# Performance work log

Hardware: AMD Instinct MI355X
Metric: run time of the kernel (lower is better)

Reference implementation:

```python
import jax, jax.numpy as jnp
import numpy as np

N = 100_000   # nodes
D = 128       # feature dim (dim_in == dim_out, residual requires it)
E = 1_600_000 # edges
T = 4         # num_layers; edge_attr (hop distance) in 1..T


def setup_inputs() -> dict:
    key = jax.random.key(0)
    k0, k1, k2, k3, k4 = jax.random.split(key, 5)
    x = jax.random.normal(k0, (N, D), dtype=jnp.float32)
    edge_index = jax.random.randint(k1, (2, E), 0, N, dtype=jnp.int32)
    edge_attr = jax.random.randint(k2, (E,), 1, T + 1, dtype=jnp.int32)  # hop k in [1, T]
    W = jax.random.normal(k3, (T, D, D), dtype=jnp.float32) * (1.0 / np.sqrt(D))
    nu = jax.random.normal(k4, (T, T), dtype=jnp.float32) * 0.1  # nu[k-1, t]
    return {"x": x, "edge_index": edge_index, "edge_attr": edge_attr, "W": W, "nu": nu}


def _gcn_edge_coef(edge_index, mask, n):
    """Symmetric GCN normalization 1/sqrt(deg_src*deg_dst) restricted to masked edges."""
    src, dst = edge_index[0], edge_index[1]
    deg_s = jax.ops.segment_sum(mask, src, num_segments=n)
    deg_d = jax.ops.segment_sum(mask, dst, num_segments=n)
    inv = lambda d: jnp.where(d > 0, jax.lax.rsqrt(jnp.maximum(d, 1.0)), 0.0)
    return mask * inv(deg_s)[src] * inv(deg_d)[dst]  # [E]


def reference(x, edge_index, edge_attr, W, nu):
    n = x.shape[0]
    T_layers = nu.shape[1]
    src, dst = edge_index[0], edge_index[1]
    # Precompute per-hop normalized edge coefficients (A(k) masks as weights -> static shapes)
    coefs = [_gcn_edge_coef(edge_index, (edge_attr == k).astype(x.dtype), n)
             for k in range(1, T_layers + 1)]
    hist = [x]  # x_t history
    for t in range(T_layers):
        acc = jnp.zeros_like(x)
        for k in range(1, t + 2):  # k = 1 .. t+1
            h = hist[t + 1 - k] @ W[k - 1]                      # [N, D] linear
            msg = h[src] * coefs[k - 1][:, None]                # gather + weight [E, D]
            agg = jax.ops.segment_sum(msg, dst, num_segments=n) # scatter-sum [N, D]
            acc = acc + nu[k - 1, t] * agg
        xt = hist[t] + jax.nn.relu(acc)                         # residual + ReLU
        # F.normalize(p=2, dim=-1), eps=1e-12 (cfg.gnn.l2norm assumed True)
        xt = xt / jnp.maximum(jnp.linalg.norm(xt, axis=-1, keepdims=True), 1e-12)
        hist.append(xt)
    return hist[-1]
```

## Files before the change

kernel.cpp:

```cpp
#include <hip/hip_runtime.h>

#define DD 128
#define NP 256
#define EB 8192

typedef float4 f4;
typedef __attribute__((ext_vector_type(8))) short bf16x8;
typedef __attribute__((ext_vector_type(4))) float f32x4;

__device__ __forceinline__ short toBf(float f) {
    unsigned u = __float_as_uint(f);
    u += 0x7fff + ((u >> 16) & 1);
    return (short)(u >> 16);
}
__device__ __forceinline__ float bf2f(unsigned short u) {
    return __uint_as_float(((unsigned)u) << 16);
}


__global__ __launch_bounds__(1024) void kA(const int* __restrict__ ei, int E, int PSZ, int nbA,
                                           int* __restrict__ cntB_D, int* __restrict__ cntB_S) {
    __shared__ int hd[NP], hs[NP];
    int tid = threadIdx.x;
    if (tid < NP) { hd[tid] = 0; hs[tid] = 0; }
    __syncthreads();
    int base = blockIdx.x * EB;
    int lim = min(base + EB, E);
    for (int e = base + tid; e < lim; e += 1024) {
        int s = ei[e], d = ei[E + e];
        atomicAdd(&hs[s / PSZ], 1);
        atomicAdd(&hd[d / PSZ], 1);
    }
    __syncthreads();
    if (tid < NP) {
        cntB_D[tid * nbA + blockIdx.x] = hd[tid];
        cntB_S[tid * nbA + blockIdx.x] = hs[tid];
    }
}

__global__ __launch_bounds__(512) void kB1(int* __restrict__ cntB_D, int* __restrict__ cntB_S,
                                           int nbA,
                                           int* __restrict__ partTotD, int* __restrict__ partTotS) {
    __shared__ int sh[512];
    int b = blockIdx.x, tid = threadIdx.x;
    int* cntB = (b < NP) ? cntB_D : cntB_S;
    int* partTot = (b < NP) ? partTotD : partTotS;
    int p = (b < NP) ? b : b - NP;
    int v = (tid < nbA) ? cntB[p * nbA + tid] : 0;
    sh[tid] = v; __syncthreads();
    for (int off = 1; off < 512; off <<= 1) {
        int add = (tid >= off) ? sh[tid - off] : 0;
        __syncthreads(); sh[tid] += add; __syncthreads();
    }
    if (tid < nbA) cntB[p * nbA + tid] = sh[tid] - v;
    if (tid == 511) partTot[p] = sh[511];
}

__global__ __launch_bounds__(512) void kB2(const int* __restrict__ partTotD,
                                           const int* __restrict__ partTotS,
                                           int* __restrict__ partStartD,
                                           int* __restrict__ partStartS, int E) {
    __shared__ int sh[512];
    int tid = threadIdx.x;
    bool isD = tid < 256;
    int idx = isD ? tid : tid - 256;
    int v = isD ? partTotD[idx] : partTotS[idx];
    sh[tid] = v; __syncthreads();
    for (int off = 1; off < 256; off <<= 1) {
        int add = (idx >= off) ? sh[tid - off] : 0;
        __syncthreads(); sh[tid] += add; __syncthreads();
    }
    if (isD) partStartD[idx] = sh[tid] - v; else partStartS[idx] = sh[tid] - v;
    if (idx == 255) { if (isD) partStartD[NP] = E; else partStartS[NP] = E; }
}

__global__ __launch_bounds__(1024) void kC(const int* __restrict__ ei, const int* __restrict__ ea,
                                           int E, int N, int T, int PSZ, int nbA,
                                           const int* __restrict__ cntB_D, const int* __restrict__ cntB_S,
                                           const int* __restrict__ partStartD,
                                           const int* __restrict__ partStartS,
                                           int2* __restrict__ binD, int* __restrict__ binS) {
    __shared__ int pd[NP], ps[NP];
    int tid = threadIdx.x, b = blockIdx.x;
    if (tid < NP) {
        pd[tid] = cntB_D[tid * nbA + b] + partStartD[tid];
        ps[tid] = cntB_S[tid * nbA + b] + partStartS[tid];
    }
    __syncthreads();
    int base = b * EB;
    int lim = min(base + EB, E);
    for (int e = base + tid; e < lim; e += 1024) {
        int s = ei[e], d = ei[E + e], k = ea[e] - 1;
        int dp = d / PSZ, sp = s / PSZ;
        int posD = atomicAdd(&pd[dp], 1);
        binD[posD] = make_int2((d - dp * PSZ) * T + k, (k << 26) | (k * N + s));
        int posS = atomicAdd(&ps[sp], 1);
        binS[posS] = (s - sp * PSZ) * T + k;
    }
}

__global__ __launch_bounds__(512) void kDE(const int2* __restrict__ binD,
                                           const int* __restrict__ binS,
                                           const int* __restrict__ partStartD,
                                           const int* __restrict__ partStartS,
                                           int N, int T, int PSZ, int M, int E,
                                           int* __restrict__ rowptr, float* __restrict__ isdD2,
                                           int* __restrict__ ep, float* __restrict__ isdS) {
    __shared__ int cnt[4096];
    __shared__ int part[512];
    int b = blockIdx.x, tid = threadIdx.x;
    int nloc = PSZ * T;
    for (int i = tid; i < nloc; i += 512) cnt[i] = 0;
    __syncthreads();
    if (b < NP) {
        int p = b;
        int b0 = partStartD[p], b1 = partStartD[p + 1];
        for (int e = b0 + tid; e < b1; e += 512) atomicAdd(&cnt[binD[e].x], 1);
        __syncthreads();
        int CH = (nloc + 511) / 512;
        int c0 = tid * CH, c1 = min(c0 + CH, nloc);
        int s = 0;
        for (int i = c0; i < c1; i++) s += cnt[i];
        part[tid] = s; __syncthreads();
        for (int off = 1; off < 512; off <<= 1) {
            int add = (tid >= off) ? part[tid - off] : 0;
            __syncthreads(); part[tid] += add; __syncthreads();
        }
        int run = ((tid == 0) ? 0 : part[tid - 1]) + b0;
        int gb_base = p * PSZ * T;
        for (int i = c0; i < c1; i++) {
            int v = cnt[i];
            cnt[i] = run;
            int gb = gb_base + i;
            if (gb < M) {
                rowptr[gb] = run;
                isdD2[gb] = rsqrtf((float)max(v, 1));
            }
            run += v;
        }
        __syncthreads();
        for (int e = b0 + tid; e < b1; e += 512) {
            int2 v = binD[e];
            int pos = atomicAdd(&cnt[v.x], 1);
            ep[pos] = v.y;
        }
        if (p == 0 && tid == 0) rowptr[M] = E;
    } else {
        int p = b - NP;
        int b0 = partStartS[p], b1 = partStartS[p + 1];
        for (int e = b0 + tid; e < b1; e += 512) atomicAdd(&cnt[binS[e]], 1);
        __syncthreads();
        int s0 = p * PSZ;
        for (int i = tid; i < nloc; i += 512) {
            int sl = i / T, k = i - sl * T;
            int snode = s0 + sl;
            if (snode < N) isdS[k * N + snode] = rsqrtf((float)max(cnt[i], 1));
        }
    }
}

__global__ void k_prepW(const float* __restrict__ W, ushort* __restrict__ WT, int tot) {
    int i = blockIdx.x * blockDim.x + threadIdx.x;
    if (i >= tot) return;
    int k = i >> 14, rem = i & 16383, j = rem >> 7, d = rem & 127;
    WT[i] = (ushort)toBf(W[(size_t)k * 16384 + (size_t)d * DD + j]);
}

__global__ void k_cvt(const float* __restrict__ x, ushort* __restrict__ xb, int n8) {
    int i = blockIdx.x * blockDim.x + threadIdx.x;
    if (i >= n8) return;
    const f4* q = (const f4*)(x + (size_t)i * 8);
    f4 lo = q[0], hi = q[1];
    bf16x8 r;
    r[0] = toBf(lo.x); r[1] = toBf(lo.y); r[2] = toBf(lo.z); r[3] = toBf(lo.w);
    r[4] = toBf(hi.x); r[5] = toBf(hi.y); r[6] = toBf(hi.z); r[7] = toBf(hi.w);
    *(bf16x8*)(xb + (size_t)i * 8) = r;
}


struct APtrs { const ushort* a0; const ushort* a1; const ushort* a2; const ushort* a3; };

__global__ __launch_bounds__(256) void k_gemm_batch(APtrs ap,
                                                    const ushort* __restrict__ WTb,
                                                    const float* __restrict__ iskb,
                                                    ushort* __restrict__ Hb, int N) {
    __shared__ ushort lW[128 * 128];
    int k0 = blockIdx.y;
    const ushort* A = (k0 == 0) ? ap.a0 : (k0 == 1) ? ap.a1 : (k0 == 2) ? ap.a2 : ap.a3;
    const ushort* WT = WTb + (size_t)k0 * DD * DD;
    const float* isk = iskb + (size_t)k0 * N;
    ushort* H = Hb + (size_t)k0 * N * DD;

    int tid = threadIdx.x;
#pragma unroll
    for (int i = 0; i < 8; i++) {
        int g = tid + i * 256;
        int row = g >> 4, slot = g & 15;
        bf16x8 v = *(const bf16x8*)(WT + row * DD + slot * 8);
        *(bf16x8*)(lW + row * DD + (slot ^ (row & 7)) * 8) = v;
    }
    __syncthreads();

    int wave = tid >> 6;
    int lane = tid & 63;
    int rlo = lane & 15;
    int khi = lane >> 4;
    int r0 = blockIdx.x * 256 + wave * 64;

    f32x4 acc[4][8];
#pragma unroll
    for (int s = 0; s < 4; s++)
#pragma unroll
        for (int j = 0; j < 8; j++) acc[s][j] = (f32x4){0.f, 0.f, 0.f, 0.f};

    int ca[4];
#pragma unroll
    for (int s = 0; s < 4; s++) {
        int r = r0 + s * 16 + rlo;
        ca[s] = r < N ? r : N - 1;
    }

#pragma unroll
    for (int kk = 0; kk < 4; kk++) {
        int d0 = kk * 32 + khi * 8;
        bf16x8 a[4];
#pragma unroll
        for (int s = 0; s < 4; s++)
            a[s] = *(const bf16x8*)(A + (size_t)ca[s] * DD + d0);
        int q = kk * 4 + khi;
#pragma unroll
        for (int cg = 0; cg < 8; cg++) {
            int row = cg * 16 + rlo;
            bf16x8 b = *(const bf16x8*)(lW + row * DD + (q ^ (rlo & 7)) * 8);
#pragma unroll
            for (int s = 0; s < 4; s++)
                acc[s][cg] = __builtin_amdgcn_mfma_f32_16x16x32_bf16(a[s], b, acc[s][cg], 0, 0, 0);
        }
    }

#pragma unroll
    for (int s = 0; s < 4; s++) {
#pragma unroll
        for (int r = 0; r < 4; r++) {
            int row = r0 + s * 16 + khi * 4 + r;
            if (row < N) {
                float sc = isk[row];
#pragma unroll
                for (int cg = 0; cg < 8; cg++)
                    H[(size_t)row * DD + cg * 16 + rlo] = (ushort)toBf(sc * acc[s][cg][r]);
            }
        }
    }
}


__device__ __forceinline__ float selw(float w0, float w1, float w2, float w3, int k) {
    float a = (k & 1) ? w1 : w0;
    float b = (k & 1) ? w3 : w2;
    return (k & 2) ? b : a;
}

__global__ __launch_bounds__(256) void k_agg_fin(
        const ushort* __restrict__ H,
        const int* __restrict__ ep,
        const int* __restrict__ rp,
        const float* __restrict__ isdD2,
        const float* __restrict__ nu, int t, int T, int nk,
        const ushort* __restrict__ hp,
        ushort* __restrict__ hnB,
        float* __restrict__ outF,
        int N) {
    int node = (blockIdx.x * blockDim.x + threadIdx.x) >> 5;
    if (node >= N) return;
    int lane = threadIdx.x & 31;
    int rbase = node * T;
    int b0 = rp[rbase], b1 = rp[rbase + nk];

    float w0 = nu[t] * isdD2[rbase];
    float w1 = (1 < nk) ? nu[T + t]     * isdD2[rbase + 1] : 0.f;
    float w2 = (2 < nk) ? nu[2 * T + t] * isdD2[rbase + 2] : 0.f;
    float w3 = (3 < nk) ? nu[3 * T + t] * isdD2[rbase + 3] : 0.f;

    const char* Hc = (const char*)H;
    unsigned lb = (unsigned)lane << 3;

    float sx = 0.f, sy = 0.f, sz = 0.f, sw = 0.f;
    int e = b0;

#define DEC(P, O, C) \
    O = ((((unsigned)(P)) & 0x3FFFFFFu) << 8) | lb; \
    C = selw(w0, w1, w2, w3, (P) >> 26);

#define ACC(G, C) { \
    float f0 = __uint_as_float((G).x << 16); \
    float f1 = __uint_as_float((G).x & 0xffff0000u); \
    float f2 = __uint_as_float((G).y << 16); \
    float f3 = __uint_as_float((G).y & 0xffff0000u); \
    sx = fmaf((C), f0, sx); sy = fmaf((C), f1, sy); \
    sz = fmaf((C), f2, sz); sw = fmaf((C), f3, sw); }

    for (; e + 7 < b1; e += 8) {
        int p0 = ep[e],     p1 = ep[e + 1], p2 = ep[e + 2], p3 = ep[e + 3];
        int p4 = ep[e + 4], p5 = ep[e + 5], p6 = ep[e + 6], p7 = ep[e + 7];
        unsigned o0, o1, o2, o3, o4, o5, o6, o7;
        float c0, c1, c2, c3, c4, c5, c6, c7;
        DEC(p0, o0, c0) DEC(p1, o1, c1) DEC(p2, o2, c2) DEC(p3, o3, c3)
        DEC(p4, o4, c4) DEC(p5, o5, c5) DEC(p6, o6, c6) DEC(p7, o7, c7)
        uint2 g0 = *(const uint2*)(Hc + o0);
        uint2 g1 = *(const uint2*)(Hc + o1);
        uint2 g2 = *(const uint2*)(Hc + o2);
        uint2 g3 = *(const uint2*)(Hc + o3);
        uint2 g4 = *(const uint2*)(Hc + o4);
        uint2 g5 = *(const uint2*)(Hc + o5);
        uint2 g6 = *(const uint2*)(Hc + o6);
        uint2 g7 = *(const uint2*)(Hc + o7);
        ACC(g0, c0) ACC(g1, c1) ACC(g2, c2) ACC(g3, c3)
        ACC(g4, c4) ACC(g5, c5) ACC(g6, c6) ACC(g7, c7)
    }
    if (e + 3 < b1) {
        int p0 = ep[e], p1 = ep[e + 1], p2 = ep[e + 2], p3 = ep[e + 3];
        unsigned o0, o1, o2, o3;
        float c0, c1, c2, c3;
        DEC(p0, o0, c0) DEC(p1, o1, c1) DEC(p2, o2, c2) DEC(p3, o3, c3)
        uint2 g0 = *(const uint2*)(Hc + o0);
        uint2 g1 = *(const uint2*)(Hc + o1);
        uint2 g2 = *(const uint2*)(Hc + o2);
        uint2 g3 = *(const uint2*)(Hc + o3);
        ACC(g0, c0) ACC(g1, c1) ACC(g2, c2) ACC(g3, c3)
        e += 4;
    }
    for (; e < b1; e++) {
        int p0 = ep[e];
        unsigned o0; float c0;
        DEC(p0, o0, c0)
        uint2 g0 = *(const uint2*)(Hc + o0);
        ACC(g0, c0)
    }
#undef DEC
#undef ACC

    unsigned nodeOff = ((unsigned)node << 8) | lb;
    uint2 hv = *(const uint2*)((const char*)hp + nodeOff);
    float vx = __uint_as_float(hv.x << 16)         + fmaxf(sx, 0.f);
    float vy = __uint_as_float(hv.x & 0xffff0000u) + fmaxf(sy, 0.f);
    float vz = __uint_as_float(hv.y << 16)         + fmaxf(sz, 0.f);
    float vw = __uint_as_float(hv.y & 0xffff0000u) + fmaxf(sw, 0.f);
    float ss = vx * vx + vy * vy + vz * vz + vw * vw;
#pragma unroll
    for (int off = 16; off; off >>= 1) ss += __shfl_xor(ss, off, 32);
    float inv = 1.f / fmaxf(sqrtf(ss), 1e-12f);
    vx *= inv; vy *= inv; vz *= inv; vw *= inv;
    if (outF) {
        f4 o; o.x = vx; o.y = vy; o.z = vz; o.w = vw;
        *(f4*)((char*)outF + (((size_t)node << 9) | ((size_t)lane << 4))) = o;
    } else {
        uint lo = ((unsigned)(unsigned short)toBf(vx)) | (((unsigned)(unsigned short)toBf(vy)) << 16);
        uint hi = ((unsigned)(unsigned short)toBf(vz)) | (((unsigned)(unsigned short)toBf(vw)) << 16);
        uint2 ob; ob.x = lo; ob.y = hi;
        *(uint2*)((char*)hnB + nodeOff) = ob;
    }
}


extern "C" void kernel_launch(void* const* d_in, const int* in_sizes, int n_in,
                              void* d_out, int out_size, void* d_ws, size_t ws_size,
                              hipStream_t stream) {
    const float* x  = (const float*)d_in[0];
    const int*   ei = (const int*)d_in[1];
    const int*   ea = (const int*)d_in[2];
    const float* W  = (const float*)d_in[3];
    const float* nu = (const float*)d_in[4];
    float* out = (float*)d_out;

    int N = in_sizes[0] / DD;
    int E = in_sizes[1] / 2;
    int T = in_sizes[3] / (DD * DD);
    int M = T * N;
    size_t ND = (size_t)N * DD;

    int PSZ = (N + NP - 1) / NP;
    if (PSZ * T > 4096) return;
    int nbA = (E + EB - 1) / EB;
    if (nbA > 512) return;

    float*  isdS  = (float*)d_ws;
    float*  isdD2 = isdS + M;
    ushort* xb    = (ushort*)(isdD2 + M);
    ushort* h1b   = xb + ND;
    ushort* h2b   = h1b + ND;
    ushort* h3b   = h2b + ND;
    ushort* Hb    = h3b + ND;
    ushort* WT    = Hb + (size_t)T * ND;
    int* rowptr   = (int*)(WT + (size_t)T * DD * DD);
    int* ep       = rowptr + M + 1;
    int2* binD       = (int2*)Hb;
    int*  binS       = (int*)(binD + E);
    int*  cntB_D     = binS + E;
    int*  cntB_S     = cntB_D + NP * nbA;
    int*  partStartD = cntB_S + NP * nbA;
    int*  partStartS = partStartD + NP + 1;
    int*  partTotD   = partStartS + NP + 1;
    int*  partTotS   = partTotD + NP;

    size_t req = sizeof(float) * 2 * (size_t)M
               + sizeof(ushort) * ((size_t)(4 + T) * ND + (size_t)T * DD * DD)
               + sizeof(int) * ((size_t)M + 1 + (size_t)E + 64);
    if (ws_size < req) return;
    size_t scratch = sizeof(int) * (3 * (size_t)E + 2 * (size_t)NP * nbA + 4 * (NP + 1));
    if (scratch > sizeof(ushort) * (size_t)T * ND) return;

    kA<<<nbA, 1024, 0, stream>>>(ei, E, PSZ, nbA, cntB_D, cntB_S);
    kB1<<<2 * NP, 512, 0, stream>>>(cntB_D, cntB_S, nbA, partTotD, partTotS);
    kB2<<<1, 512, 0, stream>>>(partTotD, partTotS, partStartD, partStartS, E);
    kC<<<nbA, 1024, 0, stream>>>(ei, ea, E, N, T, PSZ, nbA, cntB_D, cntB_S,
                                 partStartD, partStartS, binD, binS);
    kDE<<<2 * NP, 512, 0, stream>>>(binD, binS, partStartD, partStartS,
                                    N, T, PSZ, M, E, rowptr, isdD2, ep, isdS);
    k_prepW<<<(T * DD * DD + 255) / 256, 256, 0, stream>>>(W, WT, T * DD * DD);
    k_cvt<<<((int)(ND / 8) + 255) / 256, 256, 0, stream>>>(x, xb, (int)(ND / 8));

    const ushort* histB[4] = {xb, h1b, h2b, h3b};

    int nodeBlocks = ((size_t)N * 32 + 255) / 256;
    int gemmBlocks = (N + 255) / 256;

    for (int t = 0; t < T; t++) {
        APtrs ap;
        ap.a0 = histB[t];
        ap.a1 = (t >= 1) ? histB[t - 1] : histB[0];
        ap.a2 = (t >= 2) ? histB[t - 2] : histB[0];
        ap.a3 = (t >= 3) ? histB[t - 3] : histB[0];
        dim3 grid(gemmBlocks, t + 1);
        k_gemm_batch<<<grid, 256, 0, stream>>>(ap, WT, isdS, Hb, N);

        bool lastL = (t == T - 1);
        k_agg_fin<<<nodeBlocks, 256, 0, stream>>>(Hb, ep, rowptr, isdD2,
                                                  nu, t, T, t + 1, histB[t],
                                                  lastL ? nullptr : (ushort*)histB[t + 1],
                                                  lastL ? out : nullptr, N);
    }
}
```

Before: 413.1 us.

## Fuse preprocessing kernels, drop partition-scan kernel, pack bin entries tighter

Folds the W transpose and x-to-bf16 conversion into the edge-histogram kernel as extra blocks, and removes the separate partition-prefix kernel by recomputing the 256-entry scan inside kC and kDE. Destination bin entries shrink from int2 to one packed int, and source bin entries from int to ushort, which cuts scratch traffic in the CSR build. Edge blocks are halved in size so there are more of them. This removes launches and memory traffic, but the scan is repeated in every block and new limits on T*N and PSZ*T are imposed by the narrower encoding.

```diff
diff --git a/kernel.cpp b/kernel.cpp
--- a/kernel.cpp
+++ b/kernel.cpp
@@ -2,7 +2,7 @@
 
 #define DD 128
 #define NP 256
-#define EB 8192
+#define EB 4096
 
 typedef float4 f4;
 typedef __attribute__((ext_vector_type(8))) short bf16x8;
@@ -18,23 +18,45 @@
 }
 
 
-__global__ __launch_bounds__(1024) void kA(const int* __restrict__ ei, int E, int PSZ, int nbA,
-                                           int* __restrict__ cntB_D, int* __restrict__ cntB_S) {
+__global__ __launch_bounds__(1024) void kAF(const int* __restrict__ ei, int E, int PSZ, int nbA,
+                                            int* __restrict__ cntB_D, int* __restrict__ cntB_S,
+                                            const float* __restrict__ W, ushort* __restrict__ WT,
+                                            int totW, int nPW,
+                                            const float* __restrict__ x, ushort* __restrict__ xb,
+                                            int n8) {
     __shared__ int hd[NP], hs[NP];
-    int tid = threadIdx.x;
-    if (tid < NP) { hd[tid] = 0; hs[tid] = 0; }
-    __syncthreads();
-    int base = blockIdx.x * EB;
-    int lim = min(base + EB, E);
-    for (int e = base + tid; e < lim; e += 1024) {
-        int s = ei[e], d = ei[E + e];
-        atomicAdd(&hs[s / PSZ], 1);
-        atomicAdd(&hd[d / PSZ], 1);
-    }
-    __syncthreads();
-    if (tid < NP) {
-        cntB_D[tid * nbA + blockIdx.x] = hd[tid];
-        cntB_S[tid * nbA + blockIdx.x] = hs[tid];
+    int tid = threadIdx.x, b = blockIdx.x;
+    if (b < nbA) {
+        if (tid < NP) { hd[tid] = 0; hs[tid] = 0; }
+        __syncthreads();
+        int base = b * EB;
+        int lim = min(base + EB, E);
+        for (int e = base + tid; e < lim; e += 1024) {
+            int s = ei[e], d = ei[E + e];
+            atomicAdd(&hs[s / PSZ], 1);
+            atomicAdd(&hd[d / PSZ], 1);
+        }
+        __syncthreads();
+        if (tid < NP) {
+            cntB_D[tid * nbA + b] = hd[tid];
+            cntB_S[tid * nbA + b] = hs[tid];
+        }
+    } else if (b < nbA + nPW) {
+        int i = (b - nbA) * 1024 + tid;
+        if (i < totW) {
+            int k = i >> 14, rem = i & 16383, j = rem >> 7, d = rem & 127;
+            WT[i] = (ushort)toBf(W[(size_t)k * 16384 + (size_t)d * DD + j]);
+        }
+    } else {
+        int i = (b - nbA - nPW) * 1024 + tid;
+        if (i < n8) {
+            const f4* q = (const f4*)(x + (size_t)i * 8);
+            f4 lo = q[0], hi = q[1];
+            bf16x8 r;
+            r[0] = toBf(lo.x); r[1] = toBf(lo.y); r[2] = toBf(lo.z); r[3] = toBf(lo.w);
+            r[4] = toBf(hi.x); r[5] = toBf(hi.y); r[6] = toBf(hi.z); r[7] = toBf(hi.w);
+            *(bf16x8*)(xb + (size_t)i * 8) = r;
+        }
     }
 }
 
@@ -56,35 +78,27 @@
     if (tid == 511) partTot[p] = sh[511];
 }
 
-__global__ __launch_bounds__(512) void kB2(const int* __restrict__ partTotD,
-                                           const int* __restrict__ partTotS,
-                                           int* __restrict__ partStartD,
-                                           int* __restrict__ partStartS, int E) {
-    __shared__ int sh[512];
-    int tid = threadIdx.x;
-    bool isD = tid < 256;
-    int idx = isD ? tid : tid - 256;
-    int v = isD ? partTotD[idx] : partTotS[idx];
-    sh[tid] = v; __syncthreads();
-    for (int off = 1; off < 256; off <<= 1) {
-        int add = (idx >= off) ? sh[tid - off] : 0;
-        __syncthreads(); sh[tid] += add; __syncthreads();
-    }
-    if (isD) partStartD[idx] = sh[tid] - v; else partStartS[idx] = sh[tid] - v;
-    if (idx == 255) { if (isD) partStartD[NP] = E; else partStartS[NP] = E; }
-}
-
 __global__ __launch_bounds__(1024) void kC(const int* __restrict__ ei, const int* __restrict__ ea,
                                            int E, int N, int T, int PSZ, int nbA,
                                            const int* __restrict__ cntB_D, const int* __restrict__ cntB_S,
-                                           const int* __restrict__ partStartD,
-                                           const int* __restrict__ partStartS,
-                                           int2* __restrict__ binD, int* __restrict__ binS) {
+                                           const int* __restrict__ partTotD,
+                                           const int* __restrict__ partTotS,
+                                           int* __restrict__ binD, ushort* __restrict__ binS) {
     __shared__ int pd[NP], ps[NP];
+    __shared__ int sc[512];
     int tid = threadIdx.x, b = blockIdx.x;
+    if (tid < 512) sc[tid] = (tid < 256) ? partTotD[tid] : partTotS[tid - 256];
+    __syncthreads();
+    for (int off = 1; off < 256; off <<= 1) {
+        int add = 0;
+        if (tid < 512 && (tid & 255) >= off) add = sc[tid - off];
+        __syncthreads();
+        if (tid < 512) sc[tid] += add;
+        __syncthreads();
+    }
     if (tid < NP) {
-        pd[tid] = cntB_D[tid * nbA + b] + partStartD[tid];
-        ps[tid] = cntB_S[tid * nbA + b] + partStartS[tid];
+        pd[tid] = cntB_D[tid * nbA + b] + (sc[tid] - partTotD[tid]);
+        ps[tid] = cntB_S[tid * nbA + b] + (sc[tid + 256] - partTotS[tid]);
     }
     __syncthreads();
     int base = b * EB;
@@ -92,30 +106,45 @@
     for (int e = base + tid; e < lim; e += 1024) {
         int s = ei[e], d = ei[E + e], k = ea[e] - 1;
         int dp = d / PSZ, sp = s / PSZ;
+        int loc = (d - dp * PSZ) * T + k;
         int posD = atomicAdd(&pd[dp], 1);
-        binD[posD] = make_int2((d - dp * PSZ) * T + k, (k << 26) | (k * N + s));
+        binD[posD] = (loc << 21) | (k << 19) | (k * N + s);
         int posS = atomicAdd(&ps[sp], 1);
-        binS[posS] = (s - sp * PSZ) * T + k;
-    }
-}
-
-__global__ __launch_bounds__(512) void kDE(const int2* __restrict__ binD,
-                                           const int* __restrict__ binS,
-                                           const int* __restrict__ partStartD,
-                                           const int* __restrict__ partStartS,
+        binS[posS] = (ushort)((s - sp * PSZ) * T + k);
+    }
+}
+
+__global__ __launch_bounds__(512) void kDE(const int* __restrict__ binD,
+                                           const ushort* __restrict__ binS,
+                                           const int* __restrict__ partTotD,
+                                           const int* __restrict__ partTotS,
                                            int N, int T, int PSZ, int M, int E,
                                            int* __restrict__ rowptr, float* __restrict__ isdD2,
                                            int* __restrict__ ep, float* __restrict__ isdS) {
     __shared__ int cnt[4096];
     __shared__ int part[512];
+    __shared__ int sc[256];
     int b = blockIdx.x, tid = threadIdx.x;
+    bool isD = b < NP;
+    int p = isD ? b : b - NP;
+    const int* pt = isD ? partTotD : partTotS;
+    if (tid < 256) sc[tid] = pt[tid];
+    __syncthreads();
+    for (int off = 1; off < 256; off <<= 1) {
+        int add = (tid < 256 && tid >= off) ? sc[tid - off] : 0;
+        __syncthreads();
+        if (tid < 256) sc[tid] += add;
+        __syncthreads();
+    }
+    int b1 = sc[p];
+    int b0 = b1 - pt[p];
+    __syncthreads();
     int nloc = PSZ * T;
     for (int i = tid; i < nloc; i += 512) cnt[i] = 0;
     __syncthreads();
-    if (b < NP) {
-        int p = b;
-        int b0 = partStartD[p], b1 = partStartD[p + 1];
-        for (int e = b0 + tid; e < b1; e += 512) atomicAdd(&cnt[binD[e].x], 1);
+    if (isD) {
+        for (int e = b0 + tid; e < b1; e += 512)
+            atomicAdd(&cnt[((unsigned)binD[e]) >> 21], 1);
         __syncthreads();
         int CH = (nloc + 511) / 512;
         int c0 = tid * CH, c1 = min(c0 + CH, nloc);
@@ -140,15 +169,14 @@
         }
         __syncthreads();
         for (int e = b0 + tid; e < b1; e += 512) {
-            int2 v = binD[e];
-            int pos = atomicAdd(&cnt[v.x], 1);
-            ep[pos] = v.y;
+            int v = binD[e];
+            int pos = atomicAdd(&cnt[((unsigned)v) >> 21], 1);
+            ep[pos] = v & 0x1FFFFF;
         }
         if (p == 0 && tid == 0) rowptr[M] = E;
     } else {
-        int p = b - NP;
-        int b0 = partStartS[p], b1 = partStartS[p + 1];
-        for (int e = b0 + tid; e < b1; e += 512) atomicAdd(&cnt[binS[e]], 1);
+        for (int e = b0 + tid; e < b1; e += 512)
+            atomicAdd(&cnt[(int)binS[e]], 1);
         __syncthreads();
         int s0 = p * PSZ;
         for (int i = tid; i < nloc; i += 512) {
@@ -157,24 +185,6 @@
             if (snode < N) isdS[k * N + snode] = rsqrtf((float)max(cnt[i], 1));
         }
     }
-}
-
-__global__ void k_prepW(const float* __restrict__ W, ushort* __restrict__ WT, int tot) {
-    int i = blockIdx.x * blockDim.x + threadIdx.x;
-    if (i >= tot) return;
-    int k = i >> 14, rem = i & 16383, j = rem >> 7, d = rem & 127;
-    WT[i] = (ushort)toBf(W[(size_t)k * 16384 + (size_t)d * DD + j]);
-}
-
-__global__ void k_cvt(const float* __restrict__ x, ushort* __restrict__ xb, int n8) {
-    int i = blockIdx.x * blockDim.x + threadIdx.x;
-    if (i >= n8) return;
-    const f4* q = (const f4*)(x + (size_t)i * 8);
-    f4 lo = q[0], hi = q[1];
-    bf16x8 r;
-    r[0] = toBf(lo.x); r[1] = toBf(lo.y); r[2] = toBf(lo.z); r[3] = toBf(lo.w);
-    r[4] = toBf(hi.x); r[5] = toBf(hi.y); r[6] = toBf(hi.z); r[7] = toBf(hi.w);
-    *(bf16x8*)(xb + (size_t)i * 8) = r;
 }
 
 
@@ -288,8 +298,8 @@
     int e = b0;
 
 #define DEC(P, O, C) \
-    O = ((((unsigned)(P)) & 0x3FFFFFFu) << 8) | lb; \
-    C = selw(w0, w1, w2, w3, (P) >> 26);
+    O = ((((unsigned)(P)) & 0x7FFFFu) << 8) | lb; \
+    C = selw(w0, w1, w2, w3, (P) >> 19);
 
 #define ACC(G, C) { \
     float f0 = __uint_as_float((G).x << 16); \
@@ -379,7 +389,8 @@
     size_t ND = (size_t)N * DD;
 
     int PSZ = (N + NP - 1) / NP;
-    if (PSZ * T > 4096) return;
+    if (PSZ * T > 2048) return;
+    if ((long)T * N > (1L << 19)) return;
     int nbA = (E + EB - 1) / EB;
     if (nbA > 512) return;
 
@@ -393,31 +404,33 @@
     ushort* WT    = Hb + (size_t)T * ND;
     int* rowptr   = (int*)(WT + (size_t)T * DD * DD);
     int* ep       = rowptr + M + 1;
-    int2* binD       = (int2*)Hb;
-    int*  binS       = (int*)(binD + E);
-    int*  cntB_D     = binS + E;
-    int*  cntB_S     = cntB_D + NP * nbA;
-    int*  partStartD = cntB_S + NP * nbA;
-    int*  partStartS = partStartD + NP + 1;
-    int*  partTotD   = partStartS + NP + 1;
-    int*  partTotS   = partTotD + NP;
+    int*    binD     = (int*)Hb;
+    ushort* binS     = (ushort*)(binD + E);
+    int*    cntB_D   = (int*)(binS + (((size_t)E + 1) & ~(size_t)1));
+    int*    cntB_S   = cntB_D + NP * nbA;
+    int*    partTotD = cntB_S + NP * nbA;
+    int*    partTotS = partTotD + NP;
 
     size_t req = sizeof(float) * 2 * (size_t)M
                + sizeof(ushort) * ((size_t)(4 + T) * ND + (size_t)T * DD * DD)
                + sizeof(int) * ((size_t)M + 1 + (size_t)E + 64);
     if (ws_size < req) return;
-    size_t scratch = sizeof(int) * (3 * (size_t)E + 2 * (size_t)NP * nbA + 4 * (NP + 1));
+    size_t scratch = 4 * (size_t)E + 2 * ((size_t)E + 2)
+                   + sizeof(int) * (2 * (size_t)NP * nbA + 2 * NP + 16);
     if (scratch > sizeof(ushort) * (size_t)T * ND) return;
 
-    kA<<<nbA, 1024, 0, stream>>>(ei, E, PSZ, nbA, cntB_D, cntB_S);
+    int totW = T * DD * DD;
+    int nPW = (totW + 1023) / 1024;
+    int n8 = (int)(ND / 8);
+    int nCvt = (n8 + 1023) / 1024;
+
+    kAF<<<nbA + nPW + nCvt, 1024, 0, stream>>>(ei, E, PSZ, nbA, cntB_D, cntB_S,
+                                               W, WT, totW, nPW, x, xb, n8);
     kB1<<<2 * NP, 512, 0, stream>>>(cntB_D, cntB_S, nbA, partTotD, partTotS);
-    kB2<<<1, 512, 0, stream>>>(partTotD, partTotS, partStartD, partStartS, E);
     kC<<<nbA, 1024, 0, stream>>>(ei, ea, E, N, T, PSZ, nbA, cntB_D, cntB_S,
-                                 partStartD, partStartS, binD, binS);
-    kDE<<<2 * NP, 512, 0, stream>>>(binD, binS, partStartD, partStartS,
+                                 partTotD, partTotS, binD, binS);
+    kDE<<<2 * NP, 512, 0, stream>>>(binD, binS, partTotD, partTotS,
                                     N, T, PSZ, M, E, rowptr, isdD2, ep, isdS);
-    k_prepW<<<(T * DD * DD + 255) / 256, 256, 0, stream>>>(W, WT, T * DD * DD);
-    k_cvt<<<((int)(ND / 8) + 255) / 256, 256, 0, stream>>>(x, xb, (int)(ND / 8));
 
     const ushort* histB[4] = {xb, h1b, h2b, h3b};
 
```

Measured after the change: 408.7 us. No clear change (-1.1%).
